# Performance work log

Measured on AMD Instinct MI355X. Metric: run time of the kernel, lower is better.

Reference implementation:

```python
import jax, jax.numpy as jnp
import numpy as np

BS, L, H, D = 4, 1024, 12, 768   # docs, seq len, attn heads, hidden
NE, M, P = 42, 96, 42 * 42        # max entities (min_height), mentions/doc, ht pairs
OFFSET = 1                        # bert/roberta [CLS] offset


def setup_inputs() -> dict:
    key = jax.random.key(0)
    k1, k2, k3, k4, k5 = jax.random.split(key, 5)
    sequence_output = jax.random.normal(k1, (BS, L, D), jnp.float32)
    attention = jax.random.uniform(k2, (BS, H, L, L), jnp.float32)
    mention_pos = jax.random.randint(k3, (BS, M), 0, L - OFFSET - 1).astype(jnp.int32)
    mention_entity = jnp.sort(jax.random.randint(k4, (BS, M), 0, NE), axis=-1).astype(jnp.int32)
    hts = jax.random.randint(k5, (BS, P, 2), 0, NE).astype(jnp.int32)
    return {"sequence_output": sequence_output, "attention": attention,
            "mention_pos": mention_pos, "mention_entity": mention_entity, "hts": hts}


def _per_doc_entities(seq, att, pos, ent):
    # seq [L,D], att [H,L,L], pos [M] mention token idx, ent [M] entity segment id
    idx = pos + OFFSET
    m_emb = seq[idx]                              # [M,D]  gathered mention embeddings
    m_att = jnp.transpose(att[:, idx], (1, 0, 2))  # [M,H,L] gathered mention attentions
    counts = jax.ops.segment_sum(jnp.ones((M,), seq.dtype), ent, num_segments=NE)
    has = counts > 0
    # mean-pool attentions per entity (zeros for empty entities, as in torch code)
    e_att = jax.ops.segment_sum(m_att, ent, num_segments=NE) / jnp.maximum(counts, 1.0)[:, None, None]
    # stable logsumexp-pool embeddings per entity
    seg_max = jax.ops.segment_max(m_emb, ent, num_segments=NE)      # -inf for empty segments
    seg_max = jnp.where(has[:, None], seg_max, 0.0)
    seg_sum = jax.ops.segment_sum(jnp.exp(m_emb - seg_max[ent]), ent, num_segments=NE)
    e_emb = jnp.where(has[:, None], jnp.log(jnp.maximum(seg_sum, 1e-30)) + seg_max, 0.0)
    return e_emb, e_att                           # [NE,D], [NE,H,L]


def _channel_map(seq, e_att):
    # all-pairs (h_att * t_att).mean(heads), normalize over tokens, contract with seq
    pair = jnp.einsum('ahl,bhl->abl', e_att, e_att) / H      # [NE,NE,L]
    pair = pair / (pair.sum(-1, keepdims=True) + 1e-5)
    return jnp.einsum('abl,ld->abd', pair, seq)              # [NE,NE,D]


def reference(sequence_output, attention, mention_pos, mention_entity, hts):
    e_emb, e_att = jax.vmap(_per_doc_entities)(sequence_output, attention,
                                               mention_pos, mention_entity)
    hss = jax.vmap(lambda emb, ht: emb[ht[:, 0]])(e_emb, hts).reshape(BS * P, D)
    tss = jax.vmap(lambda emb, ht: emb[ht[:, 1]])(e_emb, hts).reshape(BS * P, D)
    feature_map = jax.vmap(_channel_map)(sequence_output, e_att)  # [BS,NE,NE,D]
    return hss, tss, feature_map
```

## Files before the change

kernel.cpp:

```cpp
#include <hip/hip_runtime.h>
#include <hip/hip_bf16.h>

#define BSZ   4
#define LSEQ  1024
#define NH    12
#define DDIM  768
#define NEN   42
#define NM    96
#define NPAIR (NEN*NEN)
#define OFF   1

typedef short bf16x8 __attribute__((ext_vector_type(8)));
typedef float f32x4  __attribute__((ext_vector_type(4)));

__device__ __forceinline__ float bf2f(unsigned short u) {
    union { unsigned u; float f; } c; c.u = ((unsigned)u) << 16; return c.f;
}

typedef const __attribute__((address_space(1))) unsigned int glb_u32;
typedef __attribute__((address_space(3))) unsigned int lds_u32;
__device__ __forceinline__ void glds16(const void* g, void* l) {
    __builtin_amdgcn_global_load_lds((glb_u32*)g, (lds_u32*)l, 16, 0, 0);
}

#define NLC   4
#define EMB_CNT  (BSZ*NEN*DDIM)
#define PSUM_CNT (BSZ*NLC*NPAIR)
#define EATT_CNT (BSZ*NEN*NH*LSEQ)
#define PTIL_CNT ((size_t)BSZ*NPAIR*LSEQ)

#define ATT_TOTAL (BSZ*NEN*NH)

#define TEN   6
#define NTILE 7
#define NTRIT (NTILE*(NTILE+1)/2)
#define LCHK  256
#define PAIR_BLKS (NTRIT*NLC*BSZ)
#define T_BLKS    ((LSEQ/32)*(DDIM/32)*BSZ)
#define EMB_BLKS  (BSZ*NEN*3)
#define MID2_TOTAL (PAIR_BLKS + T_BLKS + EMB_BLKS)

#define BM 128
#define BN 64
#define BK 64
#define MT 14
#define NT (DDIM/BN)
#define FMAP_BLKS (MT*NT*BSZ)
#define GATH_BLKS (BSZ*NPAIR/4)
#define TAIL_TOTAL (FMAP_BLKS + GATH_BLKS)

__global__ __launch_bounds__(256) void att_kernel(
        const float* __restrict__ att,
        const int* __restrict__ mpos,
        const int* __restrict__ ment,
        __hip_bfloat16* __restrict__ e_att) {
    __shared__ int sp[NM];
    __shared__ int se[NM];
    int id = blockIdx.x;
    int h = id % NH;
    int e = (id / NH) % NEN;
    int b = id / (NH * NEN);
    int t = threadIdx.x;
    if (t < NM) { sp[t] = mpos[b*NM + t] + OFF; se[t] = ment[b*NM + t]; }
    __syncthreads();
    const float* ab = att + ((size_t)(b*NH + h)) * LSEQ * LSEQ;
    float4 acc = {0.f, 0.f, 0.f, 0.f};
    int cnt = 0;
    for (int m = 0; m < NM; ++m) {
        if (se[m] == e) {
            ++cnt;
            float4 v = ((const float4*)(ab + (size_t)sp[m]*LSEQ))[t];
            acc.x += v.x; acc.y += v.y; acc.z += v.z; acc.w += v.w;
        }
    }
    float inv = cnt ? 1.f / (float)cnt : 0.f;
    union { ushort4 u4; __hip_bfloat16 hh[4]; } pk;
    pk.hh[0] = __float2bfloat16(acc.x * inv);
    pk.hh[1] = __float2bfloat16(acc.y * inv);
    pk.hh[2] = __float2bfloat16(acc.z * inv);
    pk.hh[3] = __float2bfloat16(acc.w * inv);
    ((ushort4*)(e_att + ((size_t)(b*NEN + e)*NH + h)*LSEQ))[t] = pk.u4;
}

__global__ __launch_bounds__(256) void mid2_kernel(
        const float* __restrict__ seq,
        const __hip_bfloat16* __restrict__ e_att,
        const int* __restrict__ mpos,
        const int* __restrict__ ment,
        __hip_bfloat16* __restrict__ ptil,
        float* __restrict__ psum,
        __hip_bfloat16* __restrict__ seqT,
        float* __restrict__ e_emb) {
    __shared__ __align__(16) char smraw[4352];
    const int bid = blockIdx.x;
    const int t = threadIdx.x;

    if (bid < PAIR_BLKS) {
        int tri = bid % NTRIT;
        int lc  = (bid / NTRIT) % NLC;
        int b   = bid / (NTRIT * NLC);
        int ta = 0, rem = tri;
        while (rem >= NTILE - ta) { rem -= NTILE - ta; ++ta; }
        int tb = ta + rem;
        int l = lc * LCHK + t;

        const __hip_bfloat16* ebase = e_att + (size_t)b*NEN*NH*LSEQ + l;
        float s[TEN][TEN];
        #pragma unroll
        for (int i = 0; i < TEN; ++i)
            #pragma unroll
            for (int j = 0; j < TEN; ++j) s[i][j] = 0.f;

        #pragma unroll 4
        for (int h = 0; h < NH; ++h) {
            float xa[TEN], xb[TEN];
            #pragma unroll
            for (int e = 0; e < TEN; ++e)
                xa[e] = bf2f(*(const unsigned short*)(ebase + ((size_t)(ta*TEN+e)*NH + h)*LSEQ));
            #pragma unroll
            for (int e = 0; e < TEN; ++e)
                xb[e] = bf2f(*(const unsigned short*)(ebase + ((size_t)(tb*TEN+e)*NH + h)*LSEQ));
            #pragma unroll
            for (int i = 0; i < TEN; ++i)
                #pragma unroll
                for (int j = 0; j < TEN; ++j)
                    s[i][j] += xa[i] * xb[j];
        }

        __hip_bfloat16* pbase = ptil + (size_t)b*NPAIR*LSEQ + l;
        #pragma unroll
        for (int i = 0; i < TEN; ++i) {
            #pragma unroll
            for (int j = 0; j < TEN; ++j) {
                union { unsigned short u; __hip_bfloat16 h; } pk;
                pk.h = __float2bfloat16(s[i][j]);
                int pa = ta*TEN + i, pb = tb*TEN + j;
                *(unsigned short*)(pbase + (size_t)(pa*NEN + pb)*LSEQ) = pk.u;
                if (ta != tb)
                    *(unsigned short*)(pbase + (size_t)(pb*NEN + pa)*LSEQ) = pk.u;
            }
        }

        int lane = t & 63, w = t >> 6;
        float (*redp)[TEN*TEN] = (float(*)[TEN*TEN])smraw;
        float keep = 0.f;
        #pragma unroll
        for (int i = 0; i < TEN; ++i) {
            #pragma unroll
            for (int j = 0; j < TEN; ++j) {
                float v = s[i][j];
                v += __shfl_xor(v,  1, 64);
                v += __shfl_xor(v,  2, 64);
                v += __shfl_xor(v,  4, 64);
                v += __shfl_xor(v,  8, 64);
                v += __shfl_xor(v, 16, 64);
                v += __shfl_xor(v, 32, 64);
                if (lane == i*TEN + j) keep = v;
            }
        }
        if (lane < TEN*TEN) redp[w][lane] = keep;
        __syncthreads();
        if (t < TEN*TEN) {
            float v = redp[0][t] + redp[1][t] + redp[2][t] + redp[3][t];
            int i = t / TEN, j = t % TEN;
            int pa = ta*TEN + i, pb = tb*TEN + j;
            float* ps = psum + ((size_t)(b*NLC + lc))*NPAIR;
            ps[pa*NEN + pb] = v;
            if (ta != tb) ps[pb*NEN + pa] = v;
        }
    } else if (bid < PAIR_BLKS + T_BLKS) {
        int id = bid - PAIR_BLKS;
        int l0 = (id % (LSEQ/32)) * 32;
        int d0 = ((id / (LSEQ/32)) % (DDIM/32)) * 32;
        int b  = id / ((LSEQ/32) * (DDIM/32));
        float (*tile)[33] = (float(*)[33])smraw;
        int l = t >> 3, dq = (t & 7) * 4;
        float4 v = *(const float4*)(seq + ((size_t)b*LSEQ + l0 + l)*DDIM + d0 + dq);
        tile[l][dq+0] = v.x; tile[l][dq+1] = v.y;
        tile[l][dq+2] = v.z; tile[l][dq+3] = v.w;
        __syncthreads();
        int d = t >> 3, lq = (t & 7) * 4;
        union { ushort4 u4; __hip_bfloat16 h[4]; } pk;
        pk.h[0] = __float2bfloat16(tile[lq+0][d]);
        pk.h[1] = __float2bfloat16(tile[lq+1][d]);
        pk.h[2] = __float2bfloat16(tile[lq+2][d]);
        pk.h[3] = __float2bfloat16(tile[lq+3][d]);
        *(ushort4*)(seqT + ((size_t)b*DDIM + d0 + d)*LSEQ + l0 + lq) = pk.u4;
    } else {
        int id = bid - PAIR_BLKS - T_BLKS;
        int chunk = id % 3;
        int e = (id / 3) % NEN;
        int b = id / (3 * NEN);
        int* sp   = (int*)smraw;
        int* se   = sp + NM;
        int* list = se + NM;
        int* pcnt = list + NM;
        if (t < NM) { sp[t] = mpos[b*NM + t] + OFF; se[t] = ment[b*NM + t]; }
        __syncthreads();
        if (t == 0) {
            int c = 0;
            for (int m = 0; m < NM; ++m) if (se[m] == e) list[c++] = sp[m];
            pcnt[0] = c;
        }
        __syncthreads();
        int cnt = pcnt[0];
        int d = chunk * 256 + t;
        const float* sq = seq + (size_t)b * LSEQ * DDIM + d;
        float mx = -1e30f;
        for (int m = 0; m < cnt; ++m) mx = fmaxf(mx, sq[(size_t)list[m] * DDIM]);
        float out = 0.f;
        if (cnt) {
            float s = 0.f;
            for (int m = 0; m < cnt; ++m) s += expf(sq[(size_t)list[m] * DDIM] - mx);
            out = logf(fmaxf(s, 1e-30f)) + mx;
        }
        e_emb[((size_t)b*NEN + e)*DDIM + d] = out;
    }
}

__global__ __launch_bounds__(256) void tail_kernel(
        const __hip_bfloat16* __restrict__ ptil,
        const __hip_bfloat16* __restrict__ seqT,
        const float* __restrict__ psum,
        const float* __restrict__ e_emb,
        const int* __restrict__ hts,
        float* __restrict__ out_h,
        float* __restrict__ out_t,
        float* __restrict__ fmap) {
    __shared__ __hip_bfloat16 As[2][BM*BK];
    __shared__ __hip_bfloat16 Bs[2][BN*BK];
    const int bid = blockIdx.x;
    const int t = threadIdx.x;

    if (bid >= FMAP_BLKS) {
        int id4  = bid - FMAP_BLKS;
        int grp  = t >> 6;
        int lane = t & 63;
        int id   = id4 * 4 + grp;
        int b    = id / NPAIR;
        int hi = hts[id*2 + 0];
        int ti = hts[id*2 + 1];
        const float4* eh = (const float4*)(e_emb + ((size_t)(b*NEN + hi))*DDIM);
        const float4* et = (const float4*)(e_emb + ((size_t)(b*NEN + ti))*DDIM);
        float4* oh = (float4*)(out_h + (size_t)id*DDIM);
        float4* ot = (float4*)(out_t + (size_t)id*DDIM);
        #pragma unroll
        for (int i = 0; i < 3; ++i) {
            oh[lane + 64*i] = eh[lane + 64*i];
            ot[lane + 64*i] = et[lane + 64*i];
        }
        return;
    }

    int tile = (bid & 7) * (FMAP_BLKS/8) + (bid >> 3);
    const int lane = t & 63;
    const int wid  = t >> 6;
    const int wr   = wid >> 1;
    const int wc   = wid & 1;
    const int bx = tile % MT, by = (tile / MT) % NT, b = tile / (MT*NT);
    const int r0 = bx * BM, c0 = by * BN;

    const char* Ab  = (const char*)(ptil + (size_t)b * NPAIR * LSEQ);
    const char* Btb = (const char*)(seqT + (size_t)b * DDIM * LSEQ);
    char* AsB = (char*)As;
    char* BsB = (char*)Bs;

    const f32x4 zero = {0.f, 0.f, 0.f, 0.f};
    f32x4 acc[4][2];
    #pragma unroll
    for (int m = 0; m < 4; ++m)
        #pragma unroll
        for (int n = 0; n < 2; ++n) acc[m][n] = zero;

    const int fr = lane & 15, kg = lane >> 4;

#define STAGE(buf, k0)                                                        \
    {                                                                         \
        _Pragma("unroll")                                                     \
        for (int i = 0; i < 4; ++i) {                                         \
            int L = wid*4096 + i*1024 + lane*16;                              \
            int r = L >> 7, beta = L & 127;                                   \
            glds16(Ab + (size_t)(r0 + r)*(LSEQ*2) + (k0)*2                    \
                      + (beta ^ ((r & 7) << 4)), AsB + (buf)*16384 + L);      \
        }                                                                     \
        _Pragma("unroll")                                                     \
        for (int i = 0; i < 2; ++i) {                                         \
            int L = wid*2048 + i*1024 + lane*16;                              \
            int c = L >> 7, beta = L & 127;                                   \
            glds16(Btb + (size_t)(c0 + c)*(LSEQ*2) + (k0)*2                   \
                      + (beta ^ ((c & 7) << 4)), BsB + (buf)*8192 + L);       \
        }                                                                     \
    }

    STAGE(0, 0);
    __syncthreads();

    int cur = 0;
    for (int ki = 0; ki < LSEQ/BK; ++ki) {
        if (ki + 1 < LSEQ/BK) STAGE(cur ^ 1, (ki + 1) * BK);

        const __hip_bfloat16* Ac = (const __hip_bfloat16*)(AsB + cur*16384);
        const __hip_bfloat16* Bc = (const __hip_bfloat16*)(BsB + cur*8192);

        #pragma unroll
        for (int ks = 0; ks < 2; ++ks) {
            bf16x8 af[4], bfv[2];
            #pragma unroll
            for (int m = 0; m < 4; ++m) {
                int R = wr*64 + m*16 + fr;
                int e0 = (ks*32 + kg*8) ^ ((R & 7) << 3);
                af[m] = *(const bf16x8*)(Ac + R*64 + e0);
            }
            #pragma unroll
            for (int n = 0; n < 2; ++n) {
                int C = wc*32 + n*16 + fr;
                int e0 = (ks*32 + kg*8) ^ ((C & 7) << 3);
                bfv[n] = *(const bf16x8*)(Bc + C*64 + e0);
            }
            #pragma unroll
            for (int m = 0; m < 4; ++m)
                #pragma unroll
                for (int n = 0; n < 2; ++n)
                    acc[m][n] = __builtin_amdgcn_mfma_f32_16x16x32_bf16(
                                    af[m], bfv[n], acc[m][n], 0, 0, 0);
        }
        __syncthreads();
        cur ^= 1;
    }

    const float* psb = psum + (size_t)b * NLC * NPAIR;
    #pragma unroll
    for (int m = 0; m < 4; ++m) {
        int lr0 = wr*64 + m*16 + kg*4;
        #pragma unroll
        for (int i = 0; i < 4; ++i) {
            int row = r0 + lr0 + i;
            if (row < NPAIR) {
                float S = psb[row] + psb[NPAIR + row]
                        + psb[2*NPAIR + row] + psb[3*NPAIR + row];
                float sc = 1.f / (S + (float)NH * 1e-5f);
                #pragma unroll
                for (int n = 0; n < 2; ++n) {
                    int col = c0 + wc*32 + n*16 + fr;
                    fmap[((size_t)b*NPAIR + row)*DDIM + col] = acc[m][n][i] * sc;
                }
            }
        }
    }
#undef STAGE
}

extern "C" void kernel_launch(void* const* d_in, const int* in_sizes, int n_in,
                              void* d_out, int out_size, void* d_ws, size_t ws_size,
                              hipStream_t stream) {
    const float* seq  = (const float*)d_in[0];
    const float* att  = (const float*)d_in[1];
    const int*   mpos = (const int*)d_in[2];
    const int*   ment = (const int*)d_in[3];
    const int*   hts  = (const int*)d_in[4];

    float* ws_f  = (float*)d_ws;
    float* e_emb = ws_f;
    float* psum  = ws_f + EMB_CNT;
    __hip_bfloat16* e_att = (__hip_bfloat16*)(ws_f + EMB_CNT + PSUM_CNT);
    __hip_bfloat16* ptil  = e_att + EATT_CNT;
    __hip_bfloat16* seqT  = ptil + PTIL_CNT;

    float* out_h = (float*)d_out;
    float* out_t = out_h + (size_t)BSZ*NPAIR*DDIM;
    float* fmap  = out_t + (size_t)BSZ*NPAIR*DDIM;

    hipLaunchKernelGGL(att_kernel, dim3(ATT_TOTAL), dim3(256), 0, stream,
                       att, mpos, ment, e_att);
    hipLaunchKernelGGL(mid2_kernel, dim3(MID2_TOTAL), dim3(256), 0, stream,
                       seq, e_att, mpos, ment, ptil, psum, seqT, e_emb);
    hipLaunchKernelGGL(tail_kernel, dim3(TAIL_TOTAL), dim3(256), 0, stream,
                       ptil, seqT, psum, e_emb, hts, out_h, out_t, fmap);
}
```

Before: 56.17 us.

## Exploit pair symmetry: compute only upper-triangular entity pairs in fmap GEMM

The pair-attention matrix is symmetric in (a,b), so only the upper-triangular 903 pairs are stored in a packed layout padded to 1024 rows. The fmap GEMM now runs over 8 row tiles instead of 14 and writes each result to both (a,b) and (b,a). This roughly halves the GEMM work and the ptil writes, at the cost of a loop-based triangular index decode in the epilogue and scattered duplicate stores. Padded rows beyond 903 are read uninitialised but are masked out.

```diff
diff --git a/kernel.cpp b/kernel.cpp
--- a/kernel.cpp
+++ b/kernel.cpp
@@ -8,6 +8,8 @@
 #define NEN   42
 #define NM    96
 #define NPAIR (NEN*NEN)
+#define NTRI  (NEN*(NEN+1)/2)
+#define PTROWS 1024
 #define OFF   1
 
 typedef short bf16x8 __attribute__((ext_vector_type(8)));
@@ -15,6 +17,12 @@
 
 __device__ __forceinline__ float bf2f(unsigned short u) {
     union { unsigned u; float f; } c; c.u = ((unsigned)u) << 16; return c.f;
+}
+
+__device__ __forceinline__ void tri2ab(int tri, int& a, int& b) {
+    int rem = tri, aa = 0;
+    while (rem >= NEN - aa) { rem -= NEN - aa; ++aa; }
+    a = aa; b = aa + rem;
 }
 
 typedef const __attribute__((address_space(1))) unsigned int glb_u32;
@@ -25,9 +33,9 @@
 
 #define NLC   4
 #define EMB_CNT  (BSZ*NEN*DDIM)
-#define PSUM_CNT (BSZ*NLC*NPAIR)
+#define PSUM_CNT (BSZ*NLC*PTROWS)
 #define EATT_CNT (BSZ*NEN*NH*LSEQ)
-#define PTIL_CNT ((size_t)BSZ*NPAIR*LSEQ)
+#define PTIL_CNT ((size_t)BSZ*PTROWS*LSEQ)
 
 #define ATT_TOTAL (BSZ*NEN*NH)
 
@@ -43,7 +51,7 @@
 #define BM 128
 #define BN 64
 #define BK 64
-#define MT 14
+#define MT 8
 #define NT (DDIM/BN)
 #define FMAP_BLKS (MT*NT*BSZ)
 #define GATH_BLKS (BSZ*NPAIR/4)
@@ -127,17 +135,17 @@
                     s[i][j] += xa[i] * xb[j];
         }
 
-        __hip_bfloat16* pbase = ptil + (size_t)b*NPAIR*LSEQ + l;
+        __hip_bfloat16* pbase = ptil + (size_t)b*PTROWS*LSEQ + l;
         #pragma unroll
         for (int i = 0; i < TEN; ++i) {
             #pragma unroll
             for (int j = 0; j < TEN; ++j) {
+                if (ta == tb && i > j) continue;
+                int pa = ta*TEN + i, pb = tb*TEN + j;
+                int tr = pa*NEN - pa*(pa-1)/2 + (pb - pa);
                 union { unsigned short u; __hip_bfloat16 h; } pk;
                 pk.h = __float2bfloat16(s[i][j]);
-                int pa = ta*TEN + i, pb = tb*TEN + j;
-                *(unsigned short*)(pbase + (size_t)(pa*NEN + pb)*LSEQ) = pk.u;
-                if (ta != tb)
-                    *(unsigned short*)(pbase + (size_t)(pb*NEN + pa)*LSEQ) = pk.u;
+                *(unsigned short*)(pbase + (size_t)tr*LSEQ) = pk.u;
             }
         }
 
@@ -161,12 +169,13 @@
         if (lane < TEN*TEN) redp[w][lane] = keep;
         __syncthreads();
         if (t < TEN*TEN) {
-            float v = redp[0][t] + redp[1][t] + redp[2][t] + redp[3][t];
             int i = t / TEN, j = t % TEN;
-            int pa = ta*TEN + i, pb = tb*TEN + j;
-            float* ps = psum + ((size_t)(b*NLC + lc))*NPAIR;
-            ps[pa*NEN + pb] = v;
-            if (ta != tb) ps[pb*NEN + pa] = v;
+            if (!(ta == tb && i > j)) {
+                float v = redp[0][t] + redp[1][t] + redp[2][t] + redp[3][t];
+                int pa = ta*TEN + i, pb = tb*TEN + j;
+                int tr = pa*NEN - pa*(pa-1)/2 + (pb - pa);
+                psum[((size_t)(b*NLC + lc))*PTROWS + tr] = v;
+            }
         }
     } else if (bid < PAIR_BLKS + T_BLKS) {
         int id = bid - PAIR_BLKS;
@@ -260,7 +269,7 @@
     const int bx = tile % MT, by = (tile / MT) % NT, b = tile / (MT*NT);
     const int r0 = bx * BM, c0 = by * BN;
 
-    const char* Ab  = (const char*)(ptil + (size_t)b * NPAIR * LSEQ);
+    const char* Ab  = (const char*)(ptil + (size_t)b * PTROWS * LSEQ);
     const char* Btb = (const char*)(seqT + (size_t)b * DDIM * LSEQ);
     char* AsB = (char*)As;
     char* BsB = (char*)Bs;
@@ -328,21 +337,25 @@
         cur ^= 1;
     }
 
-    const float* psb = psum + (size_t)b * NLC * NPAIR;
+    const float* psb = psum + (size_t)b * NLC * PTROWS;
     #pragma unroll
     for (int m = 0; m < 4; ++m) {
         int lr0 = wr*64 + m*16 + kg*4;
         #pragma unroll
         for (int i = 0; i < 4; ++i) {
-            int row = r0 + lr0 + i;
-            if (row < NPAIR) {
-                float S = psb[row] + psb[NPAIR + row]
-                        + psb[2*NPAIR + row] + psb[3*NPAIR + row];
+            int tri = r0 + lr0 + i;
+            if (tri < NTRI) {
+                int pa, pb; tri2ab(tri, pa, pb);
+                float S = psb[tri] + psb[PTROWS + tri]
+                        + psb[2*PTROWS + tri] + psb[3*PTROWS + tri];
                 float sc = 1.f / (S + (float)NH * 1e-5f);
                 #pragma unroll
                 for (int n = 0; n < 2; ++n) {
                     int col = c0 + wc*32 + n*16 + fr;
-                    fmap[((size_t)b*NPAIR + row)*DDIM + col] = acc[m][n][i] * sc;
+                    float v = acc[m][n][i] * sc;
+                    fmap[((size_t)b*NPAIR + pa*NEN + pb)*DDIM + col] = v;
+                    if (pa != pb)
+                        fmap[((size_t)b*NPAIR + pb*NEN + pa)*DDIM + col] = v;
                 }
             }
         }
```

After: 74.33 us. 32.3% more time.
